# Kernel tuning notes

Measured on AMD Instinct MI355X. Metric: run time of the kernel, lower is better.

The kernel has to match this reference:

```python
import jax, jax.numpy as jnp
import numpy as np

B, S, H, NH, L = 2, 2048, 2048, 16, 512
HD = H // NH  # head_dim = 128


def setup_inputs() -> dict:
    key = jax.random.key(0)
    k1, k2, k3, k4, k5 = jax.random.split(key, 5)
    scale = 0.02  # mimic xavier-scale init
    return {
        "q": jax.random.normal(k1, (B, S, H), dtype=jnp.float32),
        "latent_kv": jax.random.normal(k2, (B, S, L), dtype=jnp.float32),
        "Wq": jax.random.normal(k3, (H, H), dtype=jnp.float32) * scale,
        "Wkv_expand": jax.random.normal(k4, (2 * H, L), dtype=jnp.float32) * scale,
        "Wout": jax.random.normal(k5, (H, H), dtype=jnp.float32) * scale,
    }


def reference(q, latent_kv, Wq, Wkv_expand, Wout):
    b, sq, _ = q.shape
    sk = latent_kv.shape[1]
    # projections (torch Linear: x @ W.T)
    qp = q @ Wq.T                              # [B,Sq,H]
    kv = latent_kv @ Wkv_expand.T              # [B,Sk,2H]
    k, v = jnp.split(kv, 2, axis=-1)           # each [B,Sk,H]
    # split heads -> [B,NH,S,HD]
    qh = qp.reshape(b, sq, NH, HD).transpose(0, 2, 1, 3)
    kh = k.reshape(b, sk, NH, HD).transpose(0, 2, 1, 3)
    vh = v.reshape(b, sk, NH, HD).transpose(0, 2, 1, 3)
    inv_sqrt_d = 1.0 / jnp.sqrt(jnp.float32(HD))
    scores = jnp.einsum("bhqd,bhkd->bhqk", qh, kh) * inv_sqrt_d
    # causal mask (seq_q == seq_k)
    causal = jnp.tril(jnp.ones((sq, sk), dtype=bool))
    scores = jnp.where(causal, scores, jnp.finfo(scores.dtype).min)
    attn = jax.nn.softmax(scores, axis=-1)
    out = jnp.einsum("bhqk,bhkd->bhqd", attn, vh)  # [B,NH,Sq,HD]
    out = out.transpose(0, 2, 1, 3).reshape(b, sq, H)
    return out @ Wout.T
```

## Files before the change

kernel.cpp:

```cpp
#include <hip/hip_runtime.h>

#define SLEN 2048
#define NHEADS 16
#define HDIM 128

typedef __attribute__((ext_vector_type(8))) short bf16x8;
typedef __attribute__((ext_vector_type(4))) float f32x4;
typedef __attribute__((ext_vector_type(16))) float f32x16;

__device__ __forceinline__ unsigned short f2bf(float f) {
  union { float f; unsigned u; } v; v.f = f;
  unsigned r = v.u + 0x7FFFu + ((v.u >> 16) & 1u);
  return (unsigned short)(r >> 16);
}

__device__ __forceinline__ float bf2f(unsigned short h) {
  union { unsigned u; float f; } v; v.u = (unsigned)h << 16;
  return v.f;
}

__device__ __forceinline__ unsigned pkbf(float a, float b) {
  unsigned r;
  asm("v_cvt_pk_bf16_f32 %0, %1, %2" : "=v"(r) : "v"(a), "v"(b));
  return r;
}

__device__ __forceinline__ void gload16(const void* g, void* l) {
  __builtin_amdgcn_global_load_lds(
      (const __attribute__((address_space(1))) unsigned int*)g,
      (__attribute__((address_space(3))) unsigned int*)l, 16, 0, 0);
}

__global__ __launch_bounds__(256) void cvt_all(const float* __restrict__ q,
                                               const float* __restrict__ Wq,
                                               const float* __restrict__ lat,
                                               const float* __restrict__ Wkv,
                                               const float* __restrict__ Wout,
                                               unsigned short* __restrict__ qo,
                                               unsigned short* __restrict__ Wqo,
                                               unsigned short* __restrict__ lato,
                                               unsigned short* __restrict__ Wkvo,
                                               unsigned short* __restrict__ Wouto) {
  const int blk = blockIdx.x;
  const float* in;
  unsigned short* out;
  int base;
  if (blk < 4096)      { in = q;    out = qo;    base = 0; }
  else if (blk < 6144) { in = Wq;   out = Wqo;   base = 4096; }
  else if (blk < 7168) { in = lat;  out = lato;  base = 6144; }
  else if (blk < 8192) { in = Wkv;  out = Wkvo;  base = 7168; }
  else                 { in = Wout; out = Wouto; base = 8192; }
  const int i = (blk - base) * 256 + threadIdx.x;
  const float4* p = reinterpret_cast<const float4*>(in) + (size_t)i * 2;
  float4 a = p[0], b = p[1];
  uint4 o;
  o.x = (unsigned)f2bf(a.x) | ((unsigned)f2bf(a.y) << 16);
  o.y = (unsigned)f2bf(a.z) | ((unsigned)f2bf(a.w) << 16);
  o.z = (unsigned)f2bf(b.x) | ((unsigned)f2bf(b.y) << 16);
  o.w = (unsigned)f2bf(b.z) | ((unsigned)f2bf(b.w) << 16);
  reinterpret_cast<uint4*>(out)[i] = o;
}

template <bool OUT_F32>
__global__ __launch_bounds__(256, 2) void gemm_bt(const unsigned short* __restrict__ A,
                                                  const unsigned short* __restrict__ B,
                                                  void* __restrict__ Cv,
                                                  int M, int N, int K,
                                                  size_t zB, size_t zC, float scale) {
  __shared__ unsigned short As[4][128 * 32];
  __shared__ unsigned short Bs[4][128 * 32];
  const int tid = threadIdx.x;
  const int lane = tid & 63, wid = tid >> 6;
  const int g = lane >> 4, q = lane & 15;
  const int nbx = N >> 7;
  const int cpx = gridDim.x >> 3;
  const int bid = (blockIdx.x & 7) * cpx + (blockIdx.x >> 3);
  const int bx = bid % nbx, by = bid / nbx;
  const int tM = by << 7, tN = bx << 7;
  const int wm = (wid >> 1) * 64, wn = (wid & 1) * 64;
  const size_t zoff = (size_t)blockIdx.z;
  B += zoff * zB;

  const int sr = tid >> 2, sc = tid & 3;
  const int scs = sc ^ (sr & 3);
  const unsigned short* gA0 = A + (size_t)(tM + sr) * K + (scs << 3);
  const unsigned short* gA1 = A + (size_t)(tM + 64 + sr) * K + (scs << 3);
  const unsigned short* gB0 = B + (size_t)(tN + sr) * K + (scs << 3);
  const unsigned short* gB1 = B + (size_t)(tN + 64 + sr) * K + (scs << 3);

  const int nk = K >> 5;
  const int gq = g ^ (q & 3);

  auto STAGE = [&](int slot, int kt) {
    const size_t ko = (size_t)kt << 5;
    unsigned short* ad = &As[slot][0] + tid * 8;
    unsigned short* bd = &Bs[slot][0] + tid * 8;
    gload16(gA0 + ko, ad);
    gload16(gA1 + ko, ad + 2048);
    gload16(gB0 + ko, bd);
    gload16(gB1 + ko, bd + 2048);
  };

  STAGE(0, 0); STAGE(1, 1); STAGE(2, 2);

  f32x4 acc[4][4] = {};

  for (int t = 0; t < nk; ++t) {
    if (t + 2 < nk)      asm volatile("s_waitcnt vmcnt(8)" ::: "memory");
    else if (t + 1 < nk) asm volatile("s_waitcnt vmcnt(4)" ::: "memory");
    else                 asm volatile("s_waitcnt vmcnt(0)" ::: "memory");
    __builtin_amdgcn_s_barrier();
    if (t + 3 < nk) STAGE((t + 3) & 3, t + 3);

    const int s = t & 3;
    bf16x8 af[4], bfr[4];
#pragma unroll
    for (int i = 0; i < 4; ++i)
      af[i] = *(const bf16x8*)&As[s][(wm + i * 16 + q) * 32 + gq * 8];
#pragma unroll
    for (int j = 0; j < 4; ++j)
      bfr[j] = *(const bf16x8*)&Bs[s][(wn + j * 16 + q) * 32 + gq * 8];
    __builtin_amdgcn_s_setprio(1);
#pragma unroll
    for (int i = 0; i < 4; ++i)
#pragma unroll
      for (int j = 0; j < 4; ++j)
        acc[i][j] = __builtin_amdgcn_mfma_f32_16x16x32_bf16(af[i], bfr[j], acc[i][j], 0, 0, 0);
    __builtin_amdgcn_s_setprio(0);
  }

  if constexpr (OUT_F32) {
    float* C = (float*)Cv + zoff * zC;
#pragma unroll
    for (int i = 0; i < 4; ++i)
#pragma unroll
      for (int j = 0; j < 4; ++j)
#pragma unroll
        for (int r = 0; r < 4; ++r)
          C[(size_t)(tM + wm + i * 16 + g * 4 + r) * N + (tN + wn + j * 16 + q)] =
              acc[i][j][r] * scale;
  } else {
    unsigned short* C = (unsigned short*)Cv + zoff * zC;
#pragma unroll
    for (int i = 0; i < 4; ++i)
#pragma unroll
      for (int j = 0; j < 4; ++j)
#pragma unroll
        for (int r = 0; r < 4; ++r)
          C[(size_t)(tM + wm + i * 16 + g * 4 + r) * N + (tN + wn + j * 16 + q)] =
              f2bf(acc[i][j][r] * scale);
  }
}

__global__ __launch_bounds__(256, 2) void mla_attn(const unsigned short* __restrict__ Q,
                                                   const unsigned short* __restrict__ K,
                                                   const unsigned short* __restrict__ VT,
                                                   unsigned short* __restrict__ Opart,
                                                   float* __restrict__ Stats) {
  __shared__ unsigned short Ks[2][64 * 128];
  __shared__ unsigned short Vs[2][128 * 64];

  const int tid = threadIdx.x, lane = tid & 63, w = tid >> 6;
  const int q5 = lane & 31, half = lane >> 5, q7 = lane & 7;
  const int s = blockIdx.x & 1;
  const int pr = (blockIdx.x >> 1) & 7;
  const int bh = blockIdx.x >> 4;
  const int head = bh & 15, b = bh >> 4;

  const unsigned short* Kbase = K + (size_t)(b * 2048) * 2048 + head * 128;
  const unsigned short* Vbase = VT + (size_t)(b * 2048 + head * 128) * 2048;

  const int r0 = tid >> 4, c0 = tid & 15;
  const unsigned short* kS = Kbase + (size_t)r0 * 2048 + ((c0 ^ r0) << 3);
  const int d0 = tid >> 3, c3 = tid & 7;
  const unsigned short* vS = Vbase + (size_t)d0 * 2048 + ((c3 ^ (d0 & 7)) << 3);

  const int arow0 = q5 * 256;
  const int vrow0 = q5 * 128;
  const int q15 = q5 & 15;

  for (int t2 = 0; t2 < 2; ++t2) {
    const int qt = t2 ? pr : 15 - pr;
    const int kt0 = s * (qt + 1);
    const int ktN = kt0 + qt + 1;
    const int myq = qt * 128 + w * 32 + q5;
    const unsigned short* Qrow = Q + (size_t)(b * 2048 + myq) * 2048 + head * 128;

    bf16x8 qf[8];
#pragma unroll
    for (int ks = 0; ks < 8; ++ks)
      qf[ks] = *(const bf16x8*)((const char*)Qrow + ks * 32 + half * 16);

    __syncthreads();

    {
      const int kvb0 = kt0 * 64;
      unsigned short* kd = &Ks[kt0 & 1][0] + tid * 8;
      unsigned short* vd = &Vs[kt0 & 1][0] + tid * 8;
      const unsigned short* ks2 = kS + (size_t)kvb0 * 2048;
      const unsigned short* vs2 = vS + kvb0;
#pragma unroll
      for (int u = 0; u < 4; ++u) gload16(ks2 + (size_t)u * 16 * 2048, kd + u * 2048);
#pragma unroll
      for (int u = 0; u < 4; ++u) gload16(vs2 + (size_t)u * 32 * 2048, vd + u * 2048);
    }

    float m2 = -1e30f, l = 0.f;
    f32x16 o[4];
#pragma unroll
    for (int i = 0; i < 16; ++i) { o[0][i] = 0.f; o[1][i] = 0.f; o[2][i] = 0.f; o[3][i] = 0.f; }

    for (int kt = kt0; kt < ktN; ++kt) {
      const int cur = kt & 1;
      asm volatile("s_waitcnt vmcnt(4)" ::: "memory");
      __builtin_amdgcn_s_barrier();

      if (kt + 1 < ktN) {
        const int kvb2 = (kt + 1) * 64;
        unsigned short* kd = &Ks[cur ^ 1][0] + tid * 8;
        unsigned short* vd = &Vs[cur ^ 1][0] + tid * 8;
        const unsigned short* ks2 = kS + (size_t)kvb2 * 2048;
        const unsigned short* vs2 = vS + kvb2;
#pragma unroll
        for (int u = 0; u < 4; ++u) gload16(ks2 + (size_t)u * 16 * 2048, kd + u * 2048);
#pragma unroll
        for (int u = 0; u < 4; ++u) gload16(vs2 + (size_t)u * 32 * 2048, vd + u * 2048);
      }

      f32x16 st[2];
#pragma unroll
      for (int i = 0; i < 16; ++i) { st[0][i] = 0.f; st[1][i] = 0.f; }
      const char* kb = (const char*)&Ks[cur][0];
      __builtin_amdgcn_s_setprio(1);
#pragma unroll
      for (int ks = 0; ks < 8; ++ks) {
        const int cd = ks * 2 + half;
#pragma unroll
        for (int m = 0; m < 2; ++m) {
          bf16x8 kf = *(const bf16x8*)(kb + arow0 + m * 8192 + ((cd ^ q15) << 4));
          st[m] = __builtin_amdgcn_mfma_f32_32x32x16_bf16(kf, qf[ks], st[m], 0, 0, 0);
        }
      }
      __builtin_amdgcn_s_setprio(0);

      float t[32];
      const int kvb = kt * 64;
      const bool needmask = (kvb + 63 > qt * 128 + w * 32);
#pragma unroll
      for (int m = 0; m < 2; ++m)
#pragma unroll
        for (int r = 0; r < 16; ++r) {
          float sv = st[m][r];
          if (needmask) {
            const int kvloc = m * 32 + (r & 3) + 8 * (r >> 2) + 4 * half;
            sv = (kvb + kvloc <= myq) ? sv : -3e38f;
          }
          t[m * 16 + r] = sv;
        }
      float mx = fmaxf(t[0], t[1]);
#pragma unroll
      for (int i = 2; i < 32; i += 2) mx = fmaxf(fmaxf(mx, t[i]), t[i + 1]);
      mx = fmaxf(mx, __shfl_xor(mx, 32));

      if (!__all(mx <= m2 + 11.54f)) {
        const float mnew = fmaxf(m2, mx);
        const float rsc = __builtin_amdgcn_exp2f(m2 - mnew);
        m2 = mnew; l *= rsc;
#pragma unroll
        for (int r = 0; r < 16; ++r) {
          const int rowv = (r & 3) + 8 * (r >> 2) + 4 * half;
          const float f = __shfl(rsc, rowv);
          o[0][r] *= f; o[1][r] *= f; o[2][r] *= f; o[3][r] *= f;
        }
      }

      float ts = 0.f;
#pragma unroll
      for (int i = 0; i < 32; ++i) { t[i] = __builtin_amdgcn_exp2f(t[i] - m2); ts += t[i]; }
      ts += __shfl_xor(ts, 32);
      l += ts;

      unsigned wpk[2][4][2];
#pragma unroll
      for (int m = 0; m < 2; ++m)
#pragma unroll
        for (int r4 = 0; r4 < 4; ++r4) {
          wpk[m][r4][0] = pkbf(t[m * 16 + r4 * 4 + 0], t[m * 16 + r4 * 4 + 1]);
          wpk[m][r4][1] = pkbf(t[m * 16 + r4 * 4 + 2], t[m * 16 + r4 * 4 + 3]);
        }

      if (kt + 1 < ktN) asm volatile("s_waitcnt vmcnt(8)" ::: "memory");
      else              asm volatile("s_waitcnt vmcnt(0)" ::: "memory");
      __builtin_amdgcn_s_barrier();

      const char* vb = (const char*)&Vs[cur][0];
#pragma unroll
      for (int ks = 0; ks < 4; ++ks) {
        const int m = ks >> 1, i = ks & 1;
        const unsigned s0 = half ? wpk[m][2 * i][0] : wpk[m][2 * i + 1][0];
        const unsigned s1 = half ? wpk[m][2 * i][1] : wpk[m][2 * i + 1][1];
        const unsigned rv0 = (unsigned)__shfl_xor((int)s0, 32);
        const unsigned rv1 = (unsigned)__shfl_xor((int)s1, 32);
        const unsigned ow0 = half ? wpk[m][2 * i + 1][0] : wpk[m][2 * i][0];
        const unsigned ow1 = half ? wpk[m][2 * i + 1][1] : wpk[m][2 * i][1];
        union { unsigned u[4]; bf16x8 v; } fr;
        fr.u[0] = half ? rv0 : ow0;
        fr.u[1] = half ? rv1 : ow1;
        fr.u[2] = half ? ow0 : rv0;
        fr.u[3] = half ? ow1 : rv1;
        const int cd = ks * 2 + half;
        __builtin_amdgcn_s_setprio(1);
#pragma unroll
        for (int nf = 0; nf < 4; ++nf) {
          bf16x8 vf = *(const bf16x8*)(vb + vrow0 + nf * 4096 + ((cd ^ q7) << 4));
          o[nf] = __builtin_amdgcn_mfma_f32_32x32x16_bf16(fr.v, vf, o[nf], 0, 0, 0);
        }
        __builtin_amdgcn_s_setprio(0);
      }
    }

    const int set = (bh * 16 + qt) * 2 + s;
    const int base_o = set << 14;
    const int base_s = set << 8;
    if (half == 0) {
      Stats[base_s + (w * 32 + q5) * 2] = m2;
      Stats[base_s + (w * 32 + q5) * 2 + 1] = l;
    }
#pragma unroll
    for (int r = 0; r < 16; ++r) {
      const int rowv = (r & 3) + 8 * (r >> 2) + 4 * half;
      const int row = w * 32 + rowv;
#pragma unroll
      for (int nf = 0; nf < 4; ++nf)
        Opart[base_o + row * 128 + nf * 32 + q5] = f2bf(o[nf][r]);
    }
  }
}

__global__ __launch_bounds__(256) void mla_merge(const unsigned short* __restrict__ Op,
                                                 const float* __restrict__ St,
                                                 unsigned short* __restrict__ AO) {
  const int idx = blockIdx.x * 256 + threadIdx.x;
  const int rid = idx >> 4;
  const int d0 = (idx & 15) << 3;
  const int bhqt = rid >> 7;
  const int row = rid & 127;
  const int sb = bhqt << 1;
  const float m1 = St[(sb << 8) + row * 2];
  const float l1 = St[(sb << 8) + row * 2 + 1];
  const float m2 = St[(sb << 8) + 256 + row * 2];
  const float l2 = St[(sb << 8) + 256 + row * 2 + 1];
  const float M = fmaxf(m1, m2);
  const float w1 = __builtin_amdgcn_exp2f(m1 - M);
  const float w2 = __builtin_amdgcn_exp2f(m2 - M);
  const float inv = 1.0f / (w1 * l1 + w2 * l2);
  const unsigned short* p1 = Op + ((size_t)sb << 14) + row * 128 + d0;
  bf16x8 a = *(const bf16x8*)p1;
  bf16x8 c = *(const bf16x8*)(p1 + 16384);
  const int bh = bhqt >> 4, qt = bhqt & 15;
  const int head = bh & 15, b = bh >> 4;
  unsigned short outv[8];
#pragma unroll
  for (int j = 0; j < 8; ++j)
    outv[j] = f2bf((w1 * bf2f((unsigned short)a[j]) + w2 * bf2f((unsigned short)c[j])) * inv);
  unsigned short* dst = AO + ((size_t)(b * 2048 + qt * 128 + row)) * 2048 + head * 128 + d0;
  *(uint4*)dst = *(const uint4*)outv;
}

extern "C" void kernel_launch(void* const* d_in, const int* in_sizes, int n_in,
                              void* d_out, int out_size, void* d_ws, size_t ws_size,
                              hipStream_t stream) {
  const float* q    = (const float*)d_in[0];
  const float* lat  = (const float*)d_in[1];
  const float* Wq   = (const float*)d_in[2];
  const float* Wkv  = (const float*)d_in[3];
  const float* Wout = (const float*)d_in[4];

  char* ws = (char*)d_ws;
  unsigned short* qbf   = (unsigned short*)(ws);
  unsigned short* Opart = (unsigned short*)(ws);
  unsigned short* Wqbf  = (unsigned short*)(ws + 16777216);
  unsigned short* latbf = (unsigned short*)(ws + 25165824);
  unsigned short* Wkvbf = (unsigned short*)(ws + 29360128);
  unsigned short* Wobf  = (unsigned short*)(ws + 33554432);
  unsigned short* qpbf  = (unsigned short*)(ws + 41943040);
  unsigned short* Kbf   = (unsigned short*)(ws + 58720256);
  unsigned short* aobf  = (unsigned short*)(ws + 58720256);
  unsigned short* VTbf  = (unsigned short*)(ws + 75497472);
  float*          Stats = (float*)(ws + 92274688);
  unsigned short* Wvbf  = Wkvbf + (size_t)2048 * 512;

  const float SCALE_L2E = 0.12751742f;

  cvt_all<<<10240, 256, 0, stream>>>(q, Wq, lat, Wkv, Wout,
                                     qbf, Wqbf, latbf, Wkvbf, Wobf);

  gemm_bt<false><<<512, 256, 0, stream>>>(qbf, Wqbf, qpbf, 4096, 2048, 2048, 0, 0, SCALE_L2E);
  gemm_bt<false><<<512, 256, 0, stream>>>(latbf, Wkvbf, Kbf, 4096, 2048, 512, 0, 0, 1.0f);
  gemm_bt<false><<<dim3(256, 1, 2), 256, 0, stream>>>(
      Wvbf, latbf, VTbf, 2048, 2048, 512,
      (size_t)2048 * 512, (size_t)2048 * 2048, 1.0f);
  mla_attn<<<512, 256, 0, stream>>>(qpbf, Kbf, VTbf, Opart, Stats);
  mla_merge<<<4096, 256, 0, stream>>>(Opart, Stats, aobf);
  gemm_bt<true><<<512, 256, 0, stream>>>(aobf, Wobf, (float*)d_out, 4096, 2048, 2048, 0, 0, 1.0f);
}
```

Before: 222.3 us.

## Split attention KV range three ways with smaller tiles and occupancy-3 GEMM

After: 229.4 us. +3.2%, slower.

```diff
diff --git a/kernel.cpp b/kernel.cpp
--- a/kernel.cpp
+++ b/kernel.cpp
@@ -62,13 +62,13 @@
 }
 
 template <bool OUT_F32>
-__global__ __launch_bounds__(256, 2) void gemm_bt(const unsigned short* __restrict__ A,
+__global__ __launch_bounds__(256, 3) void gemm_bt(const unsigned short* __restrict__ A,
                                                   const unsigned short* __restrict__ B,
                                                   void* __restrict__ Cv,
                                                   int M, int N, int K,
                                                   size_t zB, size_t zC, float scale) {
-  __shared__ unsigned short As[4][128 * 32];
-  __shared__ unsigned short Bs[4][128 * 32];
+  __shared__ unsigned short As[3][128 * 32];
+  __shared__ unsigned short Bs[3][128 * 32];
   const int tid = threadIdx.x;
   const int lane = tid & 63, wid = tid >> 6;
   const int g = lane >> 4, q = lane & 15;
@@ -101,18 +101,20 @@
     gload16(gB1 + ko, bd + 2048);
   };
 
-  STAGE(0, 0); STAGE(1, 1); STAGE(2, 2);
+  STAGE(0, 0); STAGE(1, 1);
 
   f32x4 acc[4][4] = {};
 
+  int s = 0;
   for (int t = 0; t < nk; ++t) {
-    if (t + 2 < nk)      asm volatile("s_waitcnt vmcnt(8)" ::: "memory");
-    else if (t + 1 < nk) asm volatile("s_waitcnt vmcnt(4)" ::: "memory");
-    else                 asm volatile("s_waitcnt vmcnt(0)" ::: "memory");
+    if (t + 1 < nk) asm volatile("s_waitcnt vmcnt(4)" ::: "memory");
+    else            asm volatile("s_waitcnt vmcnt(0)" ::: "memory");
     __builtin_amdgcn_s_barrier();
-    if (t + 3 < nk) STAGE((t + 3) & 3, t + 3);
-
-    const int s = t & 3;
+    if (t + 2 < nk) {
+      int ns = s + 2; if (ns >= 3) ns -= 3;
+      STAGE(ns, t + 2);
+    }
+
     bf16x8 af[4], bfr[4];
 #pragma unroll
     for (int i = 0; i < 4; ++i)
@@ -127,6 +129,7 @@
       for (int j = 0; j < 4; ++j)
         acc[i][j] = __builtin_amdgcn_mfma_f32_16x16x32_bf16(af[i], bfr[j], acc[i][j], 0, 0, 0);
     __builtin_amdgcn_s_setprio(0);
+    s = s + 1 == 3 ? 0 : s + 1;
   }
 
   if constexpr (OUT_F32) {
@@ -152,19 +155,21 @@
   }
 }
 
-__global__ __launch_bounds__(256, 2) void mla_attn(const unsigned short* __restrict__ Q,
+__global__ __launch_bounds__(256, 3) void mla_attn(const unsigned short* __restrict__ Q,
                                                    const unsigned short* __restrict__ K,
                                                    const unsigned short* __restrict__ VT,
-                                                   unsigned short* __restrict__ Opart,
+                                                   unsigned short* __restrict__ Op0,
+                                                   unsigned short* __restrict__ Op1,
                                                    float* __restrict__ Stats) {
-  __shared__ unsigned short Ks[2][64 * 128];
-  __shared__ unsigned short Vs[2][128 * 64];
+  __shared__ unsigned short Ks[2][32 * 128];
+  __shared__ unsigned short Vs[2][128 * 32];
 
   const int tid = threadIdx.x, lane = tid & 63, w = tid >> 6;
-  const int q5 = lane & 31, half = lane >> 5, q7 = lane & 7;
-  const int s = blockIdx.x & 1;
-  const int pr = (blockIdx.x >> 1) & 7;
-  const int bh = blockIdx.x >> 4;
+  const int q5 = lane & 31, half = lane >> 5;
+  const int q15 = q5 & 15, q3 = q5 & 3;
+  const int bh = blockIdx.x / 24;
+  const int rem = blockIdx.x - bh * 24;
+  const int pr = rem / 3, s3 = rem - pr * 3;
   const int head = bh & 15, b = bh >> 4;
 
   const unsigned short* Kbase = K + (size_t)(b * 2048) * 2048 + head * 128;
@@ -172,17 +177,17 @@
 
   const int r0 = tid >> 4, c0 = tid & 15;
   const unsigned short* kS = Kbase + (size_t)r0 * 2048 + ((c0 ^ r0) << 3);
-  const int d0 = tid >> 3, c3 = tid & 7;
-  const unsigned short* vS = Vbase + (size_t)d0 * 2048 + ((c3 ^ (d0 & 7)) << 3);
+  const int d0 = tid >> 2, cv = tid & 3;
+  const unsigned short* vS = Vbase + (size_t)d0 * 2048 + ((cv ^ (d0 & 3)) << 3);
 
   const int arow0 = q5 * 256;
-  const int vrow0 = q5 * 128;
-  const int q15 = q5 & 15;
+  const int vrow0 = q5 * 64;
 
   for (int t2 = 0; t2 < 2; ++t2) {
     const int qt = t2 ? pr : 15 - pr;
-    const int kt0 = s * (qt + 1);
-    const int ktN = kt0 + qt + 1;
+    const int T = 4 * (qt + 1);
+    const int kt0 = (T * s3) / 3;
+    const int ktN = (T * (s3 + 1)) / 3;
     const int myq = qt * 128 + w * 32 + q5;
     const unsigned short* Qrow = Q + (size_t)(b * 2048 + myq) * 2048 + head * 128;
 
@@ -194,15 +199,15 @@
     __syncthreads();
 
     {
-      const int kvb0 = kt0 * 64;
+      const int kvb0 = kt0 * 32;
       unsigned short* kd = &Ks[kt0 & 1][0] + tid * 8;
       unsigned short* vd = &Vs[kt0 & 1][0] + tid * 8;
       const unsigned short* ks2 = kS + (size_t)kvb0 * 2048;
       const unsigned short* vs2 = vS + kvb0;
-#pragma unroll
-      for (int u = 0; u < 4; ++u) gload16(ks2 + (size_t)u * 16 * 2048, kd + u * 2048);
-#pragma unroll
-      for (int u = 0; u < 4; ++u) gload16(vs2 + (size_t)u * 32 * 2048, vd + u * 2048);
+      gload16(ks2, kd);
+      gload16(ks2 + (size_t)16 * 2048, kd + 2048);
+      gload16(vs2, vd);
+      gload16(vs2 + (size_t)64 * 2048, vd + 2048);
     }
 
     float m2 = -1e30f, l = 0.f;
@@ -212,54 +217,49 @@
 
     for (int kt = kt0; kt < ktN; ++kt) {
       const int cur = kt & 1;
-      asm volatile("s_waitcnt vmcnt(4)" ::: "memory");
+      asm volatile("s_waitcnt vmcnt(2)" ::: "memory");
       __builtin_amdgcn_s_barrier();
 
       if (kt + 1 < ktN) {
-        const int kvb2 = (kt + 1) * 64;
+        const int kvb2 = (kt + 1) * 32;
         unsigned short* kd = &Ks[cur ^ 1][0] + tid * 8;
         unsigned short* vd = &Vs[cur ^ 1][0] + tid * 8;
         const unsigned short* ks2 = kS + (size_t)kvb2 * 2048;
         const unsigned short* vs2 = vS + kvb2;
-#pragma unroll
-        for (int u = 0; u < 4; ++u) gload16(ks2 + (size_t)u * 16 * 2048, kd + u * 2048);
-#pragma unroll
-        for (int u = 0; u < 4; ++u) gload16(vs2 + (size_t)u * 32 * 2048, vd + u * 2048);
-      }
-
-      f32x16 st[2];
-#pragma unroll
-      for (int i = 0; i < 16; ++i) { st[0][i] = 0.f; st[1][i] = 0.f; }
+        gload16(ks2, kd);
+        gload16(ks2 + (size_t)16 * 2048, kd + 2048);
+        gload16(vs2, vd);
+        gload16(vs2 + (size_t)64 * 2048, vd + 2048);
+      }
+
+      f32x16 st;
+#pragma unroll
+      for (int i = 0; i < 16; ++i) st[i] = 0.f;
       const char* kb = (const char*)&Ks[cur][0];
       __builtin_amdgcn_s_setprio(1);
 #pragma unroll
       for (int ks = 0; ks < 8; ++ks) {
         const int cd = ks * 2 + half;
-#pragma unroll
-        for (int m = 0; m < 2; ++m) {
-          bf16x8 kf = *(const bf16x8*)(kb + arow0 + m * 8192 + ((cd ^ q15) << 4));
-          st[m] = __builtin_amdgcn_mfma_f32_32x32x16_bf16(kf, qf[ks], st[m], 0, 0, 0);
+        bf16x8 kf = *(const bf16x8*)(kb + arow0 + ((cd ^ q15) << 4));
+        st = __builtin_amdgcn_mfma_f32_32x32x16_bf16(kf, qf[ks], st, 0, 0, 0);
+      }
+      __builtin_amdgcn_s_setprio(0);
+
+      float t[16];
+      const int kvb = kt * 32;
+      const bool needmask = (kvb + 31 > qt * 128 + w * 32);
+#pragma unroll
+      for (int r = 0; r < 16; ++r) {
+        float sv = st[r];
+        if (needmask) {
+          const int kvloc = (r & 3) + 8 * (r >> 2) + 4 * half;
+          sv = (kvb + kvloc <= myq) ? sv : -3e38f;
         }
-      }
-      __builtin_amdgcn_s_setprio(0);
-
-      float t[32];
-      const int kvb = kt * 64;
-      const bool needmask = (kvb + 63 > qt * 128 + w * 32);
-#pragma unroll
-      for (int m = 0; m < 2; ++m)
-#pragma unroll
-        for (int r = 0; r < 16; ++r) {
-          float sv = st[m][r];
-          if (needmask) {
-            const int kvloc = m * 32 + (r & 3) + 8 * (r >> 2) + 4 * half;
-            sv = (kvb + kvloc <= myq) ? sv : -3e38f;
-          }
-          t[m * 16 + r] = sv;
-        }
+        t[r] = sv;
+      }
       float mx = fmaxf(t[0], t[1]);
 #pragma unroll
-      for (int i = 2; i < 32; i += 2) mx = fmaxf(fmaxf(mx, t[i]), t[i + 1]);
+      for (int i = 2; i < 16; i += 2) mx = fmaxf(fmaxf(mx, t[i]), t[i + 1]);
       mx = fmaxf(mx, __shfl_xor(mx, 32));
 
       if (!__all(mx <= m2 + 11.54f)) {
@@ -276,33 +276,30 @@
 
       float ts = 0.f;
 #pragma unroll
-      for (int i = 0; i < 32; ++i) { t[i] = __builtin_amdgcn_exp2f(t[i] - m2); ts += t[i]; }
+      for (int i = 0; i < 16; ++i) { t[i] = __builtin_amdgcn_exp2f(t[i] - m2); ts += t[i]; }
       ts += __shfl_xor(ts, 32);
       l += ts;
 
-      unsigned wpk[2][4][2];
-#pragma unroll
-      for (int m = 0; m < 2; ++m)
-#pragma unroll
-        for (int r4 = 0; r4 < 4; ++r4) {
-          wpk[m][r4][0] = pkbf(t[m * 16 + r4 * 4 + 0], t[m * 16 + r4 * 4 + 1]);
-          wpk[m][r4][1] = pkbf(t[m * 16 + r4 * 4 + 2], t[m * 16 + r4 * 4 + 3]);
-        }
-
-      if (kt + 1 < ktN) asm volatile("s_waitcnt vmcnt(8)" ::: "memory");
+      unsigned wpk[4][2];
+#pragma unroll
+      for (int r4 = 0; r4 < 4; ++r4) {
+        wpk[r4][0] = pkbf(t[r4 * 4 + 0], t[r4 * 4 + 1]);
+        wpk[r4][1] = pkbf(t[r4 * 4 + 2], t[r4 * 4 + 3]);
+      }
+
+      if (kt + 1 < ktN) asm volatile("s_waitcnt vmcnt(4)" ::: "memory");
       else              asm volatile("s_waitcnt vmcnt(0)" ::: "memory");
       __builtin_amdgcn_s_barrier();
 
       const char* vb = (const char*)&Vs[cur][0];
 #pragma unroll
-      for (int ks = 0; ks < 4; ++ks) {
-        const int m = ks >> 1, i = ks & 1;
-        const unsigned s0 = half ? wpk[m][2 * i][0] : wpk[m][2 * i + 1][0];
-        const unsigned s1 = half ? wpk[m][2 * i][1] : wpk[m][2 * i + 1][1];
+      for (int ks = 0; ks < 2; ++ks) {
+        const unsigned s0 = half ? wpk[2 * ks][0] : wpk[2 * ks + 1][0];
+        const unsigned s1 = half ? wpk[2 * ks][1] : wpk[2 * ks + 1][1];
         const unsigned rv0 = (unsigned)__shfl_xor((int)s0, 32);
         const unsigned rv1 = (unsigned)__shfl_xor((int)s1, 32);
-        const unsigned ow0 = half ? wpk[m][2 * i + 1][0] : wpk[m][2 * i][0];
-        const unsigned ow1 = half ? wpk[m][2 * i + 1][1] : wpk[m][2 * i][1];
+        const unsigned ow0 = half ? wpk[2 * ks + 1][0] : wpk[2 * ks][0];
+        const unsigned ow1 = half ? wpk[2 * ks + 1][1] : wpk[2 * ks][1];
         union { unsigned u[4]; bf16x8 v; } fr;
         fr.u[0] = half ? rv0 : ow0;
         fr.u[1] = half ? rv1 : ow1;
@@ -312,19 +309,19 @@
         __builtin_amdgcn_s_setprio(1);
 #pragma unroll
         for (int nf = 0; nf < 4; ++nf) {
-          bf16x8 vf = *(const bf16x8*)(vb + vrow0 + nf * 4096 + ((cd ^ q7) << 4));
+          bf16x8 vf = *(const bf16x8*)(vb + vrow0 + nf * 2048 + ((cd ^ q3) << 4));
           o[nf] = __builtin_amdgcn_mfma_f32_32x32x16_bf16(fr.v, vf, o[nf], 0, 0, 0);
         }
         __builtin_amdgcn_s_setprio(0);
       }
     }
 
-    const int set = (bh * 16 + qt) * 2 + s;
-    const int base_o = set << 14;
-    const int base_s = set << 8;
+    const int set = (bh * 16 + qt) * 3 + s3;
+    unsigned short* ob = (set < 1024) ? Op0 + ((size_t)set << 14)
+                                      : Op1 + ((size_t)(set - 1024) << 14);
     if (half == 0) {
-      Stats[base_s + (w * 32 + q5) * 2] = m2;
-      Stats[base_s + (w * 32 + q5) * 2 + 1] = l;
+      Stats[(set << 8) + (w * 32 + q5) * 2] = m2;
+      Stats[(set << 8) + (w * 32 + q5) * 2 + 1] = l;
     }
 #pragma unroll
     for (int r = 0; r < 16; ++r) {
@@ -332,12 +329,13 @@
       const int row = w * 32 + rowv;
 #pragma unroll
       for (int nf = 0; nf < 4; ++nf)
-        Opart[base_o + row * 128 + nf * 32 + q5] = f2bf(o[nf][r]);
+        ob[row * 128 + nf * 32 + q5] = f2bf(o[nf][r]);
     }
   }
 }
 
-__global__ __launch_bounds__(256) void mla_merge(const unsigned short* __restrict__ Op,
+__global__ __launch_bounds__(256) void mla_merge(const unsigned short* __restrict__ Op0,
+                                                 const unsigned short* __restrict__ Op1,
                                                  const float* __restrict__ St,
                                                  unsigned short* __restrict__ AO) {
   const int idx = blockIdx.x * 256 + threadIdx.x;
@@ -345,24 +343,36 @@
   const int d0 = (idx & 15) << 3;
   const int bhqt = rid >> 7;
   const int row = rid & 127;
-  const int sb = bhqt << 1;
-  const float m1 = St[(sb << 8) + row * 2];
-  const float l1 = St[(sb << 8) + row * 2 + 1];
-  const float m2 = St[(sb << 8) + 256 + row * 2];
-  const float l2 = St[(sb << 8) + 256 + row * 2 + 1];
-  const float M = fmaxf(m1, m2);
-  const float w1 = __builtin_amdgcn_exp2f(m1 - M);
-  const float w2 = __builtin_amdgcn_exp2f(m2 - M);
-  const float inv = 1.0f / (w1 * l1 + w2 * l2);
-  const unsigned short* p1 = Op + ((size_t)sb << 14) + row * 128 + d0;
-  bf16x8 a = *(const bf16x8*)p1;
-  bf16x8 c = *(const bf16x8*)(p1 + 16384);
+  const int sb = bhqt * 3;
+  float m[3], lv[3];
+#pragma unroll
+  for (int s = 0; s < 3; ++s) {
+    m[s] = St[((sb + s) << 8) + row * 2];
+    lv[s] = St[((sb + s) << 8) + row * 2 + 1];
+  }
+  const float M = fmaxf(fmaxf(m[0], m[1]), m[2]);
+  float wgt[3], den = 0.f;
+#pragma unroll
+  for (int s = 0; s < 3; ++s) { wgt[s] = __builtin_amdgcn_exp2f(m[s] - M); den += wgt[s] * lv[s]; }
+  const float inv = 1.0f / den;
+  bf16x8 pa[3];
+#pragma unroll
+  for (int s = 0; s < 3; ++s) {
+    const int set = sb + s;
+    const unsigned short* p = (set < 1024) ? Op0 + ((size_t)set << 14)
+                                           : Op1 + ((size_t)(set - 1024) << 14);
+    pa[s] = *(const bf16x8*)(p + row * 128 + d0);
+  }
   const int bh = bhqt >> 4, qt = bhqt & 15;
   const int head = bh & 15, b = bh >> 4;
   unsigned short outv[8];
 #pragma unroll
-  for (int j = 0; j < 8; ++j)
-    outv[j] = f2bf((w1 * bf2f((unsigned short)a[j]) + w2 * bf2f((unsigned short)c[j])) * inv);
+  for (int j = 0; j < 8; ++j) {
+    float acc = 0.f;
+#pragma unroll
+    for (int s = 0; s < 3; ++s) acc += wgt[s] * bf2f((unsigned short)pa[s][j]);
+    outv[j] = f2bf(acc * inv);
+  }
   unsigned short* dst = AO + ((size_t)(b * 2048 + qt * 128 + row)) * 2048 + head * 128 + d0;
   *(uint4*)dst = *(const uint4*)outv;
 }
@@ -378,7 +388,7 @@
 
   char* ws = (char*)d_ws;
   unsigned short* qbf   = (unsigned short*)(ws);
-  unsigned short* Opart = (unsigned short*)(ws);
+  unsigned short* Op0   = (unsigned short*)(ws);
   unsigned short* Wqbf  = (unsigned short*)(ws + 16777216);
   unsigned short* latbf = (unsigned short*)(ws + 25165824);
   unsigned short* Wkvbf = (unsigned short*)(ws + 29360128);
@@ -387,8 +397,9 @@
   unsigned short* Kbf   = (unsigned short*)(ws + 58720256);
   unsigned short* aobf  = (unsigned short*)(ws + 58720256);
   unsigned short* VTbf  = (unsigned short*)(ws + 75497472);
-  float*          Stats = (float*)(ws + 92274688);
   unsigned short* Wvbf  = Wkvbf + (size_t)2048 * 512;
+  unsigned short* Op1   = (unsigned short*)d_out;
+  float*          Stats = (float*)((char*)d_out + 16777216);
 
   const float SCALE_L2E = 0.12751742f;
 
@@ -400,7 +411,7 @@
   gemm_bt<false><<<dim3(256, 1, 2), 256, 0, stream>>>(
       Wvbf, latbf, VTbf, 2048, 2048, 512,
       (size_t)2048 * 512, (size_t)2048 * 2048, 1.0f);
-  mla_attn<<<512, 256, 0, stream>>>(qpbf, Kbf, VTbf, Opart, Stats);
-  mla_merge<<<4096, 256, 0, stream>>>(Opart, Stats, aobf);
+  mla_attn<<<768, 256, 0, stream>>>(qpbf, Kbf, VTbf, Op0, Op1, Stats);
+  mla_merge<<<4096, 256, 0, stream>>>(Op0, Op1, Stats, aobf);
   gemm_bt<true><<<512, 256, 0, stream>>>(aobf, Wobf, (float*)d_out, 4096, 2048, 2048, 0, 0, 1.0f);
 }
```

## Merge projection GEMMs into one launch and split attention KV range three ways

Applied to the files above, without the earlier changes.

Result: no change. 225.6 us (+1.5%).

```diff
diff --git a/kernel.cpp b/kernel.cpp
--- a/kernel.cpp
+++ b/kernel.cpp
@@ -62,24 +62,18 @@
 }
 
 template <bool OUT_F32>
-__global__ __launch_bounds__(256, 2) void gemm_bt(const unsigned short* __restrict__ A,
-                                                  const unsigned short* __restrict__ B,
-                                                  void* __restrict__ Cv,
-                                                  int M, int N, int K,
-                                                  size_t zB, size_t zC, float scale) {
-  __shared__ unsigned short As[4][128 * 32];
-  __shared__ unsigned short Bs[4][128 * 32];
+__device__ __forceinline__ void gemm_core(const unsigned short* __restrict__ A,
+                                          const unsigned short* __restrict__ B,
+                                          void* __restrict__ Cv,
+                                          int N, int K, float scale, int bid,
+                                          unsigned short* As, unsigned short* Bs) {
   const int tid = threadIdx.x;
   const int lane = tid & 63, wid = tid >> 6;
   const int g = lane >> 4, q = lane & 15;
   const int nbx = N >> 7;
-  const int cpx = gridDim.x >> 3;
-  const int bid = (blockIdx.x & 7) * cpx + (blockIdx.x >> 3);
   const int bx = bid % nbx, by = bid / nbx;
   const int tM = by << 7, tN = bx << 7;
   const int wm = (wid >> 1) * 64, wn = (wid & 1) * 64;
-  const size_t zoff = (size_t)blockIdx.z;
-  B += zoff * zB;
 
   const int sr = tid >> 2, sc = tid & 3;
   const int scs = sc ^ (sr & 3);
@@ -93,8 +87,8 @@
 
   auto STAGE = [&](int slot, int kt) {
     const size_t ko = (size_t)kt << 5;
-    unsigned short* ad = &As[slot][0] + tid * 8;
-    unsigned short* bd = &Bs[slot][0] + tid * 8;
+    unsigned short* ad = As + slot * 4096 + tid * 8;
+    unsigned short* bd = Bs + slot * 4096 + tid * 8;
     gload16(gA0 + ko, ad);
     gload16(gA1 + ko, ad + 2048);
     gload16(gB0 + ko, bd);
@@ -116,10 +110,10 @@
     bf16x8 af[4], bfr[4];
 #pragma unroll
     for (int i = 0; i < 4; ++i)
-      af[i] = *(const bf16x8*)&As[s][(wm + i * 16 + q) * 32 + gq * 8];
+      af[i] = *(const bf16x8*)&As[s * 4096 + (wm + i * 16 + q) * 32 + gq * 8];
 #pragma unroll
     for (int j = 0; j < 4; ++j)
-      bfr[j] = *(const bf16x8*)&Bs[s][(wn + j * 16 + q) * 32 + gq * 8];
+      bfr[j] = *(const bf16x8*)&Bs[s * 4096 + (wn + j * 16 + q) * 32 + gq * 8];
     __builtin_amdgcn_s_setprio(1);
 #pragma unroll
     for (int i = 0; i < 4; ++i)
@@ -130,7 +124,7 @@
   }
 
   if constexpr (OUT_F32) {
-    float* C = (float*)Cv + zoff * zC;
+    float* C = (float*)Cv;
 #pragma unroll
     for (int i = 0; i < 4; ++i)
 #pragma unroll
@@ -140,7 +134,7 @@
           C[(size_t)(tM + wm + i * 16 + g * 4 + r) * N + (tN + wn + j * 16 + q)] =
               acc[i][j][r] * scale;
   } else {
-    unsigned short* C = (unsigned short*)Cv + zoff * zC;
+    unsigned short* C = (unsigned short*)Cv;
 #pragma unroll
     for (int i = 0; i < 4; ++i)
 #pragma unroll
@@ -152,19 +146,57 @@
   }
 }
 
-__global__ __launch_bounds__(256, 2) void mla_attn(const unsigned short* __restrict__ Q,
+__global__ __launch_bounds__(256, 2) void gemm_multi(const unsigned short* __restrict__ qbf,
+                                                     const unsigned short* __restrict__ Wqbf,
+                                                     unsigned short* __restrict__ qpbf,
+                                                     const unsigned short* __restrict__ latbf,
+                                                     const unsigned short* __restrict__ Wkvbf,
+                                                     unsigned short* __restrict__ Kbf,
+                                                     const unsigned short* __restrict__ Wvbf,
+                                                     unsigned short* __restrict__ VTbf,
+                                                     float scale1) {
+  __shared__ unsigned short As[4 * 4096];
+  __shared__ unsigned short Bs[4 * 4096];
+  const int blk = blockIdx.x;
+  const unsigned short *A, *B;
+  unsigned short* C;
+  int K, segbase, segblocks;
+  float scale = 1.0f;
+  if (blk < 512)       { A = qbf;  B = Wqbf;  C = qpbf; K = 2048; scale = scale1; segbase = 0;    segblocks = 512; }
+  else if (blk < 1024) { A = latbf; B = Wkvbf; C = Kbf; K = 512;  segbase = 512;  segblocks = 512; }
+  else if (blk < 1280) { A = Wvbf; B = latbf; C = VTbf; K = 512;  segbase = 1024; segblocks = 256; }
+  else                 { A = Wvbf; B = latbf + (size_t)2048 * 512;
+                         C = VTbf + (size_t)2048 * 2048; K = 512; segbase = 1280; segblocks = 256; }
+  const int lb = blk - segbase;
+  const int cpx = segblocks >> 3;
+  const int bid = (lb & 7) * cpx + (lb >> 3);
+  gemm_core<false>(A, B, C, 2048, K, scale, bid, As, Bs);
+}
+
+__global__ __launch_bounds__(256, 2) void gemm_out(const unsigned short* __restrict__ A,
+                                                   const unsigned short* __restrict__ B,
+                                                   float* __restrict__ C) {
+  __shared__ unsigned short As[4 * 4096];
+  __shared__ unsigned short Bs[4 * 4096];
+  const int cpx = gridDim.x >> 3;
+  const int bid = (blockIdx.x & 7) * cpx + (blockIdx.x >> 3);
+  gemm_core<true>(A, B, C, 2048, 2048, 1.0f, bid, As, Bs);
+}
+
+__global__ __launch_bounds__(256, 3) void mla_attn(const unsigned short* __restrict__ Q,
                                                    const unsigned short* __restrict__ K,
                                                    const unsigned short* __restrict__ VT,
-                                                   unsigned short* __restrict__ Opart,
+                                                   unsigned short* __restrict__ Op0,
+                                                   unsigned short* __restrict__ Op1,
                                                    float* __restrict__ Stats) {
   __shared__ unsigned short Ks[2][64 * 128];
-  __shared__ unsigned short Vs[2][128 * 64];
+  __shared__ unsigned short Vs[128 * 64];
 
   const int tid = threadIdx.x, lane = tid & 63, w = tid >> 6;
   const int q5 = lane & 31, half = lane >> 5, q7 = lane & 7;
-  const int s = blockIdx.x & 1;
-  const int pr = (blockIdx.x >> 1) & 7;
-  const int bh = blockIdx.x >> 4;
+  const int bh = blockIdx.x / 24;
+  const int rem = blockIdx.x - bh * 24;
+  const int pr = rem / 3, s3 = rem - pr * 3;
   const int head = bh & 15, b = bh >> 4;
 
   const unsigned short* Kbase = K + (size_t)(b * 2048) * 2048 + head * 128;
@@ -181,8 +213,9 @@
 
   for (int t2 = 0; t2 < 2; ++t2) {
     const int qt = t2 ? pr : 15 - pr;
-    const int kt0 = s * (qt + 1);
-    const int ktN = kt0 + qt + 1;
+    const int T = 2 * (qt + 1);
+    const int kt0 = (T * s3) / 3;
+    const int ktN = (T * (s3 + 1)) / 3;
     const int myq = qt * 128 + w * 32 + q5;
     const unsigned short* Qrow = Q + (size_t)(b * 2048 + myq) * 2048 + head * 128;
 
@@ -194,15 +227,10 @@
     __syncthreads();
 
     {
-      const int kvb0 = kt0 * 64;
       unsigned short* kd = &Ks[kt0 & 1][0] + tid * 8;
-      unsigned short* vd = &Vs[kt0 & 1][0] + tid * 8;
-      const unsigned short* ks2 = kS + (size_t)kvb0 * 2048;
-      const unsigned short* vs2 = vS + kvb0;
+      const unsigned short* ks2 = kS + (size_t)(kt0 * 64) * 2048;
 #pragma unroll
       for (int u = 0; u < 4; ++u) gload16(ks2 + (size_t)u * 16 * 2048, kd + u * 2048);
-#pragma unroll
-      for (int u = 0; u < 4; ++u) gload16(vs2 + (size_t)u * 32 * 2048, vd + u * 2048);
     }
 
     float m2 = -1e30f, l = 0.f;
@@ -212,19 +240,20 @@
 
     for (int kt = kt0; kt < ktN; ++kt) {
       const int cur = kt & 1;
-      asm volatile("s_waitcnt vmcnt(4)" ::: "memory");
+      asm volatile("s_waitcnt vmcnt(0)" ::: "memory");
       __builtin_amdgcn_s_barrier();
 
+      {
+        unsigned short* vd = &Vs[0] + tid * 8;
+        const unsigned short* vs2 = vS + kt * 64;
+#pragma unroll
+        for (int u = 0; u < 4; ++u) gload16(vs2 + (size_t)u * 32 * 2048, vd + u * 2048);
+      }
       if (kt + 1 < ktN) {
-        const int kvb2 = (kt + 1) * 64;
         unsigned short* kd = &Ks[cur ^ 1][0] + tid * 8;
-        unsigned short* vd = &Vs[cur ^ 1][0] + tid * 8;
-        const unsigned short* ks2 = kS + (size_t)kvb2 * 2048;
-        const unsigned short* vs2 = vS + kvb2;
+        const unsigned short* ks2 = kS + (size_t)((kt + 1) * 64) * 2048;
 #pragma unroll
         for (int u = 0; u < 4; ++u) gload16(ks2 + (size_t)u * 16 * 2048, kd + u * 2048);
-#pragma unroll
-        for (int u = 0; u < 4; ++u) gload16(vs2 + (size_t)u * 32 * 2048, vd + u * 2048);
       }
 
       f32x16 st[2];
@@ -289,11 +318,11 @@
           wpk[m][r4][1] = pkbf(t[m * 16 + r4 * 4 + 2], t[m * 16 + r4 * 4 + 3]);
         }
 
-      if (kt + 1 < ktN) asm volatile("s_waitcnt vmcnt(8)" ::: "memory");
+      if (kt + 1 < ktN) asm volatile("s_waitcnt vmcnt(4)" ::: "memory");
       else              asm volatile("s_waitcnt vmcnt(0)" ::: "memory");
       __builtin_amdgcn_s_barrier();
 
-      const char* vb = (const char*)&Vs[cur][0];
+      const char* vb = (const char*)&Vs[0];
 #pragma unroll
       for (int ks = 0; ks < 4; ++ks) {
         const int m = ks >> 1, i = ks & 1;
@@ -319,12 +348,12 @@
       }
     }
 
-    const int set = (bh * 16 + qt) * 2 + s;
-    const int base_o = set << 14;
-    const int base_s = set << 8;
+    const int set = (bh * 16 + qt) * 3 + s3;
+    unsigned short* ob = (set < 1024) ? Op0 + ((size_t)set << 14)
+                                      : Op1 + ((size_t)(set - 1024) << 14);
     if (half == 0) {
-      Stats[base_s + (w * 32 + q5) * 2] = m2;
-      Stats[base_s + (w * 32 + q5) * 2 + 1] = l;
+      Stats[(set << 8) + (w * 32 + q5) * 2] = m2;
+      Stats[(set << 8) + (w * 32 + q5) * 2 + 1] = l;
     }
 #pragma unroll
     for (int r = 0; r < 16; ++r) {
@@ -332,12 +361,13 @@
       const int row = w * 32 + rowv;
 #pragma unroll
       for (int nf = 0; nf < 4; ++nf)
-        Opart[base_o + row * 128 + nf * 32 + q5] = f2bf(o[nf][r]);
+        ob[row * 128 + nf * 32 + q5] = f2bf(o[nf][r]);
     }
   }
 }
 
-__global__ __launch_bounds__(256) void mla_merge(const unsigned short* __restrict__ Op,
+__global__ __launch_bounds__(256) void mla_merge(const unsigned short* __restrict__ Op0,
+                                                 const unsigned short* __restrict__ Op1,
                                                  const float* __restrict__ St,
                                                  unsigned short* __restrict__ AO) {
   const int idx = blockIdx.x * 256 + threadIdx.x;
@@ -345,24 +375,36 @@
   const int d0 = (idx & 15) << 3;
   const int bhqt = rid >> 7;
   const int row = rid & 127;
-  const int sb = bhqt << 1;
-  const float m1 = St[(sb << 8) + row * 2];
-  const float l1 = St[(sb << 8) + row * 2 + 1];
-  const float m2 = St[(sb << 8) + 256 + row * 2];
-  const float l2 = St[(sb << 8) + 256 + row * 2 + 1];
-  const float M = fmaxf(m1, m2);
-  const float w1 = __builtin_amdgcn_exp2f(m1 - M);
-  const float w2 = __builtin_amdgcn_exp2f(m2 - M);
-  const float inv = 1.0f / (w1 * l1 + w2 * l2);
-  const unsigned short* p1 = Op + ((size_t)sb << 14) + row * 128 + d0;
-  bf16x8 a = *(const bf16x8*)p1;
-  bf16x8 c = *(const bf16x8*)(p1 + 16384);
+  const int sb = bhqt * 3;
+  float m[3], lv[3];
+#pragma unroll
+  for (int s = 0; s < 3; ++s) {
+    m[s] = St[((sb + s) << 8) + row * 2];
+    lv[s] = St[((sb + s) << 8) + row * 2 + 1];
+  }
+  const float M = fmaxf(fmaxf(m[0], m[1]), m[2]);
+  float wgt[3], den = 0.f;
+#pragma unroll
+  for (int s = 0; s < 3; ++s) { wgt[s] = __builtin_amdgcn_exp2f(m[s] - M); den += wgt[s] * lv[s]; }
+  const float inv = 1.0f / den;
+  bf16x8 pa[3];
+#pragma unroll
+  for (int s = 0; s < 3; ++s) {
+    const int set = sb + s;
+    const unsigned short* p = (set < 1024) ? Op0 + ((size_t)set << 14)
+                                           : Op1 + ((size_t)(set - 1024) << 14);
+    pa[s] = *(const bf16x8*)(p + row * 128 + d0);
+  }
   const int bh = bhqt >> 4, qt = bhqt & 15;
   const int head = bh & 15, b = bh >> 4;
   unsigned short outv[8];
 #pragma unroll
-  for (int j = 0; j < 8; ++j)
-    outv[j] = f2bf((w1 * bf2f((unsigned short)a[j]) + w2 * bf2f((unsigned short)c[j])) * inv);
+  for (int j = 0; j < 8; ++j) {
+    float acc = 0.f;
+#pragma unroll
+    for (int s = 0; s < 3; ++s) acc += wgt[s] * bf2f((unsigned short)pa[s][j]);
+    outv[j] = f2bf(acc * inv);
+  }
   unsigned short* dst = AO + ((size_t)(b * 2048 + qt * 128 + row)) * 2048 + head * 128 + d0;
   *(uint4*)dst = *(const uint4*)outv;
 }
@@ -378,7 +420,7 @@
 
   char* ws = (char*)d_ws;
   unsigned short* qbf   = (unsigned short*)(ws);
-  unsigned short* Opart = (unsigned short*)(ws);
+  unsigned short* Op0   = (unsigned short*)(ws);
   unsigned short* Wqbf  = (unsigned short*)(ws + 16777216);
   unsigned short* latbf = (unsigned short*)(ws + 25165824);
   unsigned short* Wkvbf = (unsigned short*)(ws + 29360128);
@@ -387,20 +429,18 @@
   unsigned short* Kbf   = (unsigned short*)(ws + 58720256);
   unsigned short* aobf  = (unsigned short*)(ws + 58720256);
   unsigned short* VTbf  = (unsigned short*)(ws + 75497472);
-  float*          Stats = (float*)(ws + 92274688);
   unsigned short* Wvbf  = Wkvbf + (size_t)2048 * 512;
+  unsigned short* Op1   = (unsigned short*)d_out;
+  float*          Stats = (float*)((char*)d_out + 16777216);
 
   const float SCALE_L2E = 0.12751742f;
 
   cvt_all<<<10240, 256, 0, stream>>>(q, Wq, lat, Wkv, Wout,
                                      qbf, Wqbf, latbf, Wkvbf, Wobf);
 
-  gemm_bt<false><<<512, 256, 0, stream>>>(qbf, Wqbf, qpbf, 4096, 2048, 2048, 0, 0, SCALE_L2E);
-  gemm_bt<false><<<512, 256, 0, stream>>>(latbf, Wkvbf, Kbf, 4096, 2048, 512, 0, 0, 1.0f);
-  gemm_bt<false><<<dim3(256, 1, 2), 256, 0, stream>>>(
-      Wvbf, latbf, VTbf, 2048, 2048, 512,
-      (size_t)2048 * 512, (size_t)2048 * 2048, 1.0f);
-  mla_attn<<<512, 256, 0, stream>>>(qpbf, Kbf, VTbf, Opart, Stats);
-  mla_merge<<<4096, 256, 0, stream>>>(Opart, Stats, aobf);
-  gemm_bt<true><<<512, 256, 0, stream>>>(aobf, Wobf, (float*)d_out, 4096, 2048, 2048, 0, 0, 1.0f);
-}
+  gemm_multi<<<1536, 256, 0, stream>>>(qbf, Wqbf, qpbf, latbf, Wkvbf, Kbf,
+                                       Wvbf, VTbf, SCALE_L2E);
+  mla_attn<<<768, 256, 0, stream>>>(qpbf, Kbf, VTbf, Op0, Op1, Stats);
+  mla_merge<<<4096, 256, 0, stream>>>(Op0, Op1, Stats, aobf);
+  gemm_out<<<512, 256, 0, stream>>>(aobf, Wobf, (float*)d_out);
+}
```
